# Performance work log

Measured on AMD Instinct MI355X. Metric: run time of the kernel, lower is better.

## Reference

```python
import jax, jax.numpy as jnp
import numpy as np

B, T, N = 128, 32, 196
E = 1024   # embed dim
FD = 1024  # feature dim
H = 1024   # hidden size
A = 1024   # attention dim
SCALE = 0.02


def setup_inputs() -> dict:
    key = jax.random.key(0)
    ks = jax.random.split(key, 16)
    g = lambda k, shape: (jax.random.normal(k, shape, dtype=jnp.float32) * SCALE)
    return {
        "feats": jax.random.normal(ks[0], (B, N, FD), dtype=jnp.float32),
        "embeddings": jax.random.normal(ks[1], (B, T, E), dtype=jnp.float32),
        # additive attention params: v^T tanh(feats @ Wf + h @ Wh + b_att)
        "Wf": g(ks[2], (FD, A)),
        "Wh": g(ks[3], (H, A)),
        "b_att": jnp.zeros((A,), dtype=jnp.float32),
        "v": g(ks[4], (A,)),
        # layer-0 LSTMCell (input = concat(embed, attn) of size E+FD)
        "W_ih0": g(ks[5], (4 * H, E + FD)),
        "W_hh0": g(ks[6], (4 * H, H)),
        "b_ih0": jnp.zeros((4 * H,), dtype=jnp.float32),
        "b_hh0": jnp.zeros((4 * H,), dtype=jnp.float32),
        # layer-1 LSTMCell (input size H)
        "W_ih1": g(ks[7], (4 * H, H)),
        "W_hh1": g(ks[8], (4 * H, H)),
        "b_ih1": jnp.zeros((4 * H,), dtype=jnp.float32),
        "b_hh1": jnp.zeros((4 * H,), dtype=jnp.float32),
    }


def _lstm_cell(x, h, c, W_ih, W_hh, b_ih, b_hh):
    # PyTorch LSTMCell: gates ordered i, f, g, o
    gates = x @ W_ih.T + h @ W_hh.T + (b_ih + b_hh)
    i, f, g, o = jnp.split(gates, 4, axis=-1)
    c_new = jax.nn.sigmoid(f) * c + jax.nn.sigmoid(i) * jnp.tanh(g)
    h_new = jax.nn.sigmoid(o) * jnp.tanh(c_new)
    return h_new, c_new


def reference(feats, embeddings, Wf, Wh, b_att, v, W_ih0, W_hh0, b_ih0, b_hh0,
              W_ih1, W_hh1, b_ih1, b_hh1):
    Bb = embeddings.shape[0]
    # precompute the h-independent half of the attention energies: [B, N, A]
    f_proj = jnp.einsum("bnf,fa->bna", feats, Wf) + b_att

    h0 = jnp.zeros((Bb, H), dtype=feats.dtype)
    c0 = jnp.zeros((Bb, H), dtype=feats.dtype)

    def step(carry, embed_t):
        h0, c0 = carry
        # additive attention with query h0
        e = jnp.tanh(f_proj + (h0 @ Wh)[:, None, :])      # [B, N, A]
        scores = jnp.einsum("bna,a->bn", e, v)            # [B, N]
        alpha = jax.nn.softmax(scores, axis=-1)
        attn = jnp.einsum("bn,bnf->bf", alpha, feats)     # [B, FD]
        x = jnp.concatenate([embed_t, attn], axis=1)      # [B, E+FD]
        h0n, c0n = _lstm_cell(x, h0, c0, W_ih0, W_hh0, b_ih0, b_hh0)
        # faithful to source: layer 1 uses (h0n, c0n) as its state AND h0n as input
        h1, c1 = _lstm_cell(h0n, h0n, c0n, W_ih1, W_hh1, b_ih1, b_hh1)
        return (h0n, c0n), h1

    (_, _), outs = jax.lax.scan(step, (h0, c0), jnp.swapaxes(embeddings, 0, 1))
    return jnp.swapaxes(outs, 0, 1)  # [B, T, H]
```

## Files before the change

kernel.cpp:

```cpp
#include <hip/hip_runtime.h>
#include <cstddef>

typedef unsigned short ushort_t;
typedef unsigned int uint_t;
typedef __attribute__((ext_vector_type(8))) short bf16x8;
typedef __attribute__((ext_vector_type(4))) float f32x4;

constexpr int kB  = 128;
constexpr int kT  = 32;
constexpr int kN  = 196;
constexpr int kH  = 1024;

__device__ __forceinline__ float fsigmoid(float x) { return 1.f / (1.f + __expf(-x)); }
__device__ __forceinline__ float ftanh(float x)    { return 1.f - 2.f / (__expf(2.f * x) + 1.f); }
__device__ __forceinline__ ushort_t f2bf(float f) {
    uint_t u = __float_as_uint(f);
    return (ushort_t)((u + 0x7fffu + ((u >> 16) & 1u)) >> 16);
}

__global__ __launch_bounds__(256) void wf_transpose(
    const float* __restrict__ Wsrc, ushort_t* __restrict__ dst)
{
    __shared__ float t[64][65];
    const int k0 = blockIdx.x * 64, a0 = blockIdx.y * 64;
    const int c = threadIdx.x & 15, r0 = threadIdx.x >> 4;
#pragma unroll
    for (int i = 0; i < 4; ++i) {
        const int r = r0 + i * 16;
        const float4 v = *(const float4*)(Wsrc + (size_t)(k0 + r) * 1024 + a0 + c * 4);
        t[r][c * 4 + 0] = v.x; t[r][c * 4 + 1] = v.y;
        t[r][c * 4 + 2] = v.z; t[r][c * 4 + 3] = v.w;
    }
    __syncthreads();
#pragma unroll
    for (int i = 0; i < 4; ++i) {
        const int r = r0 + i * 16;
        ushort4 h;
        h.x = f2bf(t[c * 4 + 0][r]); h.y = f2bf(t[c * 4 + 1][r]);
        h.z = f2bf(t[c * 4 + 2][r]); h.w = f2bf(t[c * 4 + 3][r]);
        *(ushort4*)&dst[(size_t)(a0 + r) * 1024 + k0 + c * 4] = h;
    }
}

__global__ __launch_bounds__(256) void pack_whh0(
    const float* __restrict__ Whh0, ushort_t* __restrict__ Wbig)
{
    const int idx = blockIdx.x * 256 + threadIdx.x;
    const int j = idx >> 8, k4 = (idx & 255) * 4;
    const int u = j >> 2, g = j & 3;
    const float4 v = *(const float4*)(Whh0 + (size_t)(g * 1024 + u) * 1024 + k4);
    ushort4 h;
    h.x = f2bf(v.x); h.y = f2bf(v.y); h.z = f2bf(v.z); h.w = f2bf(v.w);
    *(ushort4*)&Wbig[(size_t)(1024 + j) * 1024 + k4] = h;
}

__global__ __launch_bounds__(256) void pack_w1sum(
    const float* __restrict__ Wih1, const float* __restrict__ Whh1,
    ushort_t* __restrict__ Wbig)
{
    const int idx = blockIdx.x * 256 + threadIdx.x;
    const int j = idx >> 8, k4 = (idx & 255) * 4;
    const int u = j >> 2, g = j & 3;
    const size_t o = (size_t)(g * 1024 + u) * 1024 + k4;
    const float4 a = *(const float4*)(Wih1 + o);
    const float4 b = *(const float4*)(Whh1 + o);
    ushort4 h;
    h.x = f2bf(a.x + b.x); h.y = f2bf(a.y + b.y);
    h.z = f2bf(a.z + b.z); h.w = f2bf(a.w + b.w);
    *(ushort4*)&Wbig[(size_t)(5120 + j) * 1024 + k4] = h;
}

__global__ __launch_bounds__(256) void pack_w0cat(
    const float* __restrict__ Wih0, ushort_t* __restrict__ W0cat)
{
    const int idx = blockIdx.x * 256 + threadIdx.x;
    const int j = idx >> 9, k4 = (idx & 511) * 4;
    const int u = j >> 2, g = j & 3;
    const int srccol = (k4 < 1024) ? (k4 + 1024) : (k4 - 1024);
    const float4 v = *(const float4*)(Wih0 + (size_t)(g * 1024 + u) * 2048 + srccol);
    ushort4 h;
    h.x = f2bf(v.x); h.y = f2bf(v.y); h.z = f2bf(v.z); h.w = f2bf(v.w);
    *(ushort4*)&W0cat[(size_t)j * 2048 + k4] = h;
}

__global__ __launch_bounds__(256) void cast_bf(
    const float* __restrict__ src, ushort_t* __restrict__ dst)
{
    const size_t idx = ((size_t)blockIdx.x * 256 + threadIdx.x) * 4;
    const float4 v = *(const float4*)(src + idx);
    ushort4 h;
    h.x = f2bf(v.x); h.y = f2bf(v.y); h.z = f2bf(v.z); h.w = f2bf(v.w);
    *(ushort4*)&dst[idx] = h;
}

template<int BF>
__global__ __launch_bounds__(256) void fproj_mfma(
    const float* __restrict__ featsf, const ushort_t* __restrict__ featsbf,
    const ushort_t* __restrict__ WfT,
    const float* __restrict__ bias, ushort_t* __restrict__ fprojbf)
{
    __shared__ ushort_t As[2][128 * 40];
    __shared__ ushort_t Bs[2][128 * 40];

    const int tid = threadIdx.x;
    const int n0 = blockIdx.x * 128, m0 = blockIdx.y * 128;
    const int lane = tid & 63, w = tid >> 6;
    const int wm = (w & 1) * 64, wn = (w >> 1) * 64;
    const int lr = lane & 15, quad = lane >> 4;

    const int xrow0 = tid >> 2, xrow1 = 64 + (tid >> 2);
    const int xkc = (tid & 3) * 8;

    f32x4 acc[4][4];
#pragma unroll
    for (int i = 0; i < 4; ++i)
#pragma unroll
        for (int j = 0; j < 4; ++j)
            acc[i][j] = (f32x4){0.f, 0.f, 0.f, 0.f};

    uint4 a0r, a1r, b0r, b1r;
    float4 f00, f01, f10, f11;

    auto LOAD = [&](int k0) {
        if (BF) {
            a0r = *(const uint4*)&featsbf[(size_t)(m0 + xrow0) * 1024 + k0 + xkc];
            a1r = *(const uint4*)&featsbf[(size_t)(m0 + xrow1) * 1024 + k0 + xkc];
        } else {
            f00 = *(const float4*)&featsf[(size_t)(m0 + xrow0) * 1024 + k0 + xkc];
            f01 = *(const float4*)&featsf[(size_t)(m0 + xrow0) * 1024 + k0 + xkc + 4];
            f10 = *(const float4*)&featsf[(size_t)(m0 + xrow1) * 1024 + k0 + xkc];
            f11 = *(const float4*)&featsf[(size_t)(m0 + xrow1) * 1024 + k0 + xkc + 4];
        }
        b0r = *(const uint4*)&WfT[(size_t)(n0 + xrow0) * 1024 + k0 + xkc];
        b1r = *(const uint4*)&WfT[(size_t)(n0 + xrow1) * 1024 + k0 + xkc];
    };
    auto WRITE = [&](int buf) {
        if (BF) {
            *(uint4*)&As[buf][xrow0 * 40 + xkc] = a0r;
            *(uint4*)&As[buf][xrow1 * 40 + xkc] = a1r;
        } else {
            ushort4 h;
            h.x = f2bf(f00.x); h.y = f2bf(f00.y); h.z = f2bf(f00.z); h.w = f2bf(f00.w);
            *(ushort4*)&As[buf][xrow0 * 40 + xkc] = h;
            h.x = f2bf(f01.x); h.y = f2bf(f01.y); h.z = f2bf(f01.z); h.w = f2bf(f01.w);
            *(ushort4*)&As[buf][xrow0 * 40 + xkc + 4] = h;
            h.x = f2bf(f10.x); h.y = f2bf(f10.y); h.z = f2bf(f10.z); h.w = f2bf(f10.w);
            *(ushort4*)&As[buf][xrow1 * 40 + xkc] = h;
            h.x = f2bf(f11.x); h.y = f2bf(f11.y); h.z = f2bf(f11.z); h.w = f2bf(f11.w);
            *(ushort4*)&As[buf][xrow1 * 40 + xkc + 4] = h;
        }
        *(uint4*)&Bs[buf][xrow0 * 40 + xkc] = b0r;
        *(uint4*)&Bs[buf][xrow1 * 40 + xkc] = b1r;
    };

    LOAD(0); WRITE(0); __syncthreads();
    int cur = 0;
    for (int k0 = 32; k0 <= 1024; k0 += 32) {
        const bool more = (k0 < 1024);
        if (more) LOAD(k0);
        bf16x8 af[4], bb[4];
#pragma unroll
        for (int mf = 0; mf < 4; ++mf)
            af[mf] = *(const bf16x8*)&As[cur][(wm + mf * 16 + lr) * 40 + quad * 8];
#pragma unroll
        for (int nf = 0; nf < 4; ++nf)
            bb[nf] = *(const bf16x8*)&Bs[cur][(wn + nf * 16 + lr) * 40 + quad * 8];
#pragma unroll
        for (int mf = 0; mf < 4; ++mf)
#pragma unroll
            for (int nf = 0; nf < 4; ++nf)
                acc[mf][nf] = __builtin_amdgcn_mfma_f32_16x16x32_bf16(
                    af[mf], bb[nf], acc[mf][nf], 0, 0, 0);
        if (more) WRITE(cur ^ 1);
        __syncthreads();
        cur ^= 1;
    }

#pragma unroll
    for (int nf = 0; nf < 4; ++nf) {
        const int n = n0 + wn + nf * 16 + lr;
        const float bn = bias[n];
#pragma unroll
        for (int mf = 0; mf < 4; ++mf) {
#pragma unroll
            for (int r = 0; r < 4; ++r) {
                const int m = m0 + wm + mf * 16 + quad * 4 + r;
                fprojbf[(size_t)m * 1024 + n] = f2bf(acc[mf][nf][r] + bn);
            }
        }
    }
}

__global__ __launch_bounds__(256) void hgemm_A(
    const ushort_t* __restrict__ hbf, const ushort_t* __restrict__ Wbig,
    const float* __restrict__ cbuf,
    const float* __restrict__ bih1, const float* __restrict__ bhh1,
    float* __restrict__ hwh, float* __restrict__ Ypart,
    float* __restrict__ out, int tstep)
{
    __shared__ ushort_t xs[2][128 * 40];
    __shared__ ushort_t wsB[2][64 * 40];
    __shared__ float eps[128][65];

    const int tid = threadIdx.x;
    const int n0 = blockIdx.x * 64;
    const int lane = tid & 63, w = tid >> 6;
    const int wm = (w & 1) * 64, wn = (w >> 1) * 32;
    const int lr = lane & 15, quad = lane >> 4;

    const int xrow0 = tid >> 2, xrow1 = 64 + (tid >> 2);
    const int xkc = (tid & 3) * 8;

    f32x4 acc[4][2];
#pragma unroll
    for (int i = 0; i < 4; ++i) {
        acc[i][0] = (f32x4){0.f, 0.f, 0.f, 0.f};
        acc[i][1] = (f32x4){0.f, 0.f, 0.f, 0.f};
    }

    uint4 x0r, x1r, w0r;
    auto LOAD = [&](int k0) {
        x0r = *(const uint4*)&hbf[(size_t)xrow0 * 1024 + k0 + xkc];
        x1r = *(const uint4*)&hbf[(size_t)xrow1 * 1024 + k0 + xkc];
        w0r = *(const uint4*)&Wbig[(size_t)(n0 + xrow0) * 1024 + k0 + xkc];
    };
    auto WRITE = [&](int buf) {
        *(uint4*)&xs[buf][xrow0 * 40 + xkc] = x0r;
        *(uint4*)&xs[buf][xrow1 * 40 + xkc] = x1r;
        *(uint4*)&wsB[buf][xrow0 * 40 + xkc] = w0r;
    };

    LOAD(0); WRITE(0); __syncthreads();
    int cur = 0;
    for (int k0 = 32; k0 <= 1024; k0 += 32) {
        const bool more = (k0 < 1024);
        if (more) LOAD(k0);
        bf16x8 af[4], bb[2];
#pragma unroll
        for (int mf = 0; mf < 4; ++mf)
            af[mf] = *(const bf16x8*)&xs[cur][(wm + mf * 16 + lr) * 40 + quad * 8];
#pragma unroll
        for (int nf = 0; nf < 2; ++nf)
            bb[nf] = *(const bf16x8*)&wsB[cur][(wn + nf * 16 + lr) * 40 + quad * 8];
#pragma unroll
        for (int mf = 0; mf < 4; ++mf)
#pragma unroll
            for (int nf = 0; nf < 2; ++nf)
                acc[mf][nf] = __builtin_amdgcn_mfma_f32_16x16x32_bf16(
                    af[mf], bb[nf], acc[mf][nf], 0, 0, 0);
        if (more) WRITE(cur ^ 1);
        __syncthreads();
        cur ^= 1;
    }

    if (n0 < 5120) {
        float* dst = (n0 < 1024) ? hwh : Ypart;
        const int stride = (n0 < 1024) ? 1024 : 4096;
        const int nbase = (n0 < 1024) ? n0 : (n0 - 1024);
#pragma unroll
        for (int mf = 0; mf < 4; ++mf)
#pragma unroll
            for (int nf = 0; nf < 2; ++nf)
#pragma unroll
                for (int r = 0; r < 4; ++r) {
                    const int m = wm + mf * 16 + quad * 4 + r;
                    const int n = nbase + wn + nf * 16 + lr;
                    dst[(size_t)m * stride + n] = acc[mf][nf][r];
                }
    } else {
#pragma unroll
        for (int mf = 0; mf < 4; ++mf)
#pragma unroll
            for (int nf = 0; nf < 2; ++nf)
#pragma unroll
                for (int r = 0; r < 4; ++r)
                    eps[wm + mf * 16 + quad * 4 + r][wn + nf * 16 + lr] = acc[mf][nf][r];
        __syncthreads();
        if (tstep >= 1) {
#pragma unroll
            for (int i = 0; i < 8; ++i) {
                const int cid = i * 256 + tid;
                const int b = cid & 127, ulc = cid >> 7;
                const int u = ((n0 - 5120) >> 2) + ulc;
                const float iv = fsigmoid(eps[b][ulc * 4 + 0] + bih1[u]        + bhh1[u]);
                const float fv = fsigmoid(eps[b][ulc * 4 + 1] + bih1[1024 + u] + bhh1[1024 + u]);
                const float gv = ftanh   (eps[b][ulc * 4 + 2] + bih1[2048 + u] + bhh1[2048 + u]);
                const float ov = fsigmoid(eps[b][ulc * 4 + 3] + bih1[3072 + u] + bhh1[3072 + u]);
                const float cp = cbuf[(size_t)b * 1024 + u];
                const float cn = fv * cp + iv * gv;
                out[((size_t)b * kT + (tstep - 1)) * 1024 + u] = ov * ftanh(cn);
            }
        }
    }
}

__global__ __launch_bounds__(256) void scores_kernel(
    const ushort_t* __restrict__ fprojbf, const float* __restrict__ hwh,
    const float* __restrict__ vvec, float* __restrict__ scoresbuf)
{
    const int b = blockIdx.x, chunk = blockIdx.y;
    const int tid = threadIdx.x, lane = tid & 63, w = tid >> 6;

    float hw[16], vr[16];
    {
        const int a0 = lane * 16;
#pragma unroll
        for (int q = 0; q < 4; ++q) {
            const float4 s0 = *(const float4*)(hwh + (size_t)b * 1024 + a0 + q * 4);
            hw[q * 4 + 0] = s0.x; hw[q * 4 + 1] = s0.y;
            hw[q * 4 + 2] = s0.z; hw[q * 4 + 3] = s0.w;
            const float4 vv = *(const float4*)(vvec + a0 + q * 4);
            vr[q * 4 + 0] = vv.x; vr[q * 4 + 1] = vv.y;
            vr[q * 4 + 2] = vv.z; vr[q * 4 + 3] = vv.w;
        }
    }

#pragma unroll
    for (int i = 0; i < 7; ++i) {
        const int n = chunk * 28 + w * 7 + i;
        const ushort_t* fp = fprojbf + ((size_t)(b * kN + n)) * 1024 + lane * 16;
        const uint4 u0 = *(const uint4*)(fp);
        const uint4 u1 = *(const uint4*)(fp + 8);
        float p = 0.f;
        const uint_t uu[8] = {u0.x, u0.y, u0.z, u0.w, u1.x, u1.y, u1.z, u1.w};
#pragma unroll
        for (int q = 0; q < 8; ++q) {
            const float xa = __uint_as_float(uu[q] << 16);
            const float xb = __uint_as_float(uu[q] & 0xffff0000u);
            p += ftanh(xa + hw[2 * q]) * vr[2 * q];
            p += ftanh(xb + hw[2 * q + 1]) * vr[2 * q + 1];
        }
#pragma unroll
        for (int off = 32; off; off >>= 1) p += __shfl_down(p, off);
        if (lane == 0) scoresbuf[b * kN + n] = p;
    }
}

template<int BF>
__global__ __launch_bounds__(256) void attn_kernel(
    const float* __restrict__ scoresbuf, const float* __restrict__ featsf,
    const ushort_t* __restrict__ featsbf, ushort_t* __restrict__ attnbf)
{
    __shared__ float alpha_s[200];
    __shared__ float red[8];
    const int b = blockIdx.x;
    const int tid = threadIdx.x;

    const float val = (tid < kN) ? scoresbuf[b * kN + tid] : -1e30f;
    float m = val;
#pragma unroll
    for (int off = 32; off; off >>= 1) m = fmaxf(m, __shfl_down(m, off));
    if ((tid & 63) == 0) red[tid >> 6] = m;
    __syncthreads();
    m = fmaxf(fmaxf(red[0], red[1]), fmaxf(red[2], red[3]));
    const float e = (tid < kN) ? __expf(val - m) : 0.f;
    float s = e;
#pragma unroll
    for (int off = 32; off; off >>= 1) s += __shfl_down(s, off);
    if ((tid & 63) == 0) red[4 + (tid >> 6)] = s;
    __syncthreads();
    s = red[4] + red[5] + red[6] + red[7];
    if (tid < kN) alpha_s[tid] = e * (1.f / s);
    __syncthreads();

    if (BF) {
        const int f0 = blockIdx.y * 512 + tid * 2;
        const ushort_t* fb = featsbf + (size_t)b * kN * 1024 + f0;
        float a0 = 0.f, a1 = 0.f;
#pragma unroll 4
        for (int n = 0; n < kN; ++n) {
            const uint_t u = *(const uint_t*)(fb + (size_t)n * 1024);
            a0 += alpha_s[n] * __uint_as_float(u << 16);
            a1 += alpha_s[n] * __uint_as_float(u & 0xffff0000u);
        }
        uint_t o = ((uint_t)f2bf(a1) << 16) | (uint_t)f2bf(a0);
        *(uint_t*)&attnbf[(size_t)b * 1024 + f0] = o;
    } else {
        const int f = blockIdx.y * 256 + tid;
        const float* fb = featsf + (size_t)b * kN * 1024 + f;
        float a = 0.f;
#pragma unroll 4
        for (int n = 0; n < kN; ++n) a += alpha_s[n] * fb[(size_t)n * 1024];
        attnbf[(size_t)b * 1024 + f] = f2bf(a);
    }
}

__global__ __launch_bounds__(256) void gatesC(
    const ushort_t* __restrict__ attnbf, const ushort_t* __restrict__ embbf,
    const ushort_t* __restrict__ W0cat, const float* __restrict__ Ypart,
    const float* __restrict__ bih0, const float* __restrict__ bhh0,
    float* __restrict__ cbuf, ushort_t* __restrict__ hbf, int tstep)
{
    __shared__ ushort_t xs[2][128 * 40];
    __shared__ ushort_t ws2[2][32 * 40];
    __shared__ float eps[128][33];

    const int tid = threadIdx.x;
    const int n0 = blockIdx.x * 32;
    const int lane = tid & 63, w = tid >> 6;
    const int wm = (w & 1) * 64, wn = (w >> 1) * 16;
    const int lr = lane & 15, quad = lane >> 4;

    const int xrow0 = tid >> 2, xrow1 = 64 + (tid >> 2);
    const int xkc = (tid & 3) * 8;
    const int wrow = tid >> 3, wkc = (tid & 7) * 4;

    f32x4 acc[4];
#pragma unroll
    for (int i = 0; i < 4; ++i) acc[i] = (f32x4){0.f, 0.f, 0.f, 0.f};

    uint4 x0r, x1r; uint2 w0r;
    auto LOAD = [&](int k0) {
        const ushort_t* s0 = (k0 < 1024)
            ? (attnbf + (size_t)xrow0 * 1024 + k0)
            : (embbf + ((size_t)xrow0 * kT + tstep) * 1024 + (k0 - 1024));
        const ushort_t* s1 = (k0 < 1024)
            ? (attnbf + (size_t)xrow1 * 1024 + k0)
            : (embbf + ((size_t)xrow1 * kT + tstep) * 1024 + (k0 - 1024));
        x0r = *(const uint4*)(s0 + xkc);
        x1r = *(const uint4*)(s1 + xkc);
        w0r = *(const uint2*)&W0cat[(size_t)(n0 + wrow) * 2048 + k0 + wkc];
    };
    auto WRITE = [&](int buf) {
        *(uint4*)&xs[buf][xrow0 * 40 + xkc] = x0r;
        *(uint4*)&xs[buf][xrow1 * 40 + xkc] = x1r;
        *(uint2*)&ws2[buf][wrow * 40 + wkc] = w0r;
    };

    LOAD(0); WRITE(0); __syncthreads();
    int cur = 0;
    for (int k0 = 32; k0 <= 2048; k0 += 32) {
        const bool more = (k0 < 2048);
        if (more) LOAD(k0);
        bf16x8 af[4], bb;
#pragma unroll
        for (int mf = 0; mf < 4; ++mf)
            af[mf] = *(const bf16x8*)&xs[cur][(wm + mf * 16 + lr) * 40 + quad * 8];
        bb = *(const bf16x8*)&ws2[cur][(wn + lr) * 40 + quad * 8];
#pragma unroll
        for (int mf = 0; mf < 4; ++mf)
            acc[mf] = __builtin_amdgcn_mfma_f32_16x16x32_bf16(
                af[mf], bb, acc[mf], 0, 0, 0);
        if (more) WRITE(cur ^ 1);
        __syncthreads();
        cur ^= 1;
    }

#pragma unroll
    for (int mf = 0; mf < 4; ++mf)
#pragma unroll
        for (int r = 0; r < 4; ++r)
            eps[wm + mf * 16 + quad * 4 + r][wn + lr] = acc[mf][r];
    __syncthreads();

#pragma unroll
    for (int i = 0; i < 4; ++i) {
        const int cid = i * 256 + tid;
        const int b = cid & 127, ulc = cid >> 7;
        const int u = (n0 >> 2) + ulc;
        const int jb = n0 + ulc * 4;
        const float* yp = Ypart + (size_t)b * 4096 + jb;
        const float iv = fsigmoid(eps[b][ulc * 4 + 0] + yp[0] + bih0[u]        + bhh0[u]);
        const float fv = fsigmoid(eps[b][ulc * 4 + 1] + yp[1] + bih0[1024 + u] + bhh0[1024 + u]);
        const float gv = ftanh   (eps[b][ulc * 4 + 2] + yp[2] + bih0[2048 + u] + bhh0[2048 + u]);
        const float ov = fsigmoid(eps[b][ulc * 4 + 3] + yp[3] + bih0[3072 + u] + bhh0[3072 + u]);
        const float cp = cbuf[(size_t)b * 1024 + u];
        const float cn = fv * cp + iv * gv;
        cbuf[(size_t)b * 1024 + u] = cn;
        hbf[(size_t)b * 1024 + u] = f2bf(ov * ftanh(cn));
    }
}

extern "C" void kernel_launch(void* const* d_in, const int* in_sizes, int n_in,
                              void* d_out, int out_size, void* d_ws, size_t ws_size,
                              hipStream_t stream)
{
    const float* feats = (const float*)d_in[0];
    const float* emb   = (const float*)d_in[1];
    const float* Wf    = (const float*)d_in[2];
    const float* Wh    = (const float*)d_in[3];
    const float* b_att = (const float*)d_in[4];
    const float* vvec  = (const float*)d_in[5];
    const float* Wih0  = (const float*)d_in[6];
    const float* Whh0  = (const float*)d_in[7];
    const float* bih0  = (const float*)d_in[8];
    const float* bhh0  = (const float*)d_in[9];
    const float* Wih1  = (const float*)d_in[10];
    const float* Whh1  = (const float*)d_in[11];
    const float* bih1  = (const float*)d_in[12];
    const float* bhh1  = (const float*)d_in[13];
    float* out = (float*)d_out;

    ushort_t* fprojbf = (ushort_t*)d_ws;
    ushort_t* embbf   = fprojbf + (size_t)25088 * 1024;
    ushort_t* Wbig    = embbf   + (size_t)4096 * 1024;
    ushort_t* W0cat   = Wbig    + (size_t)9216 * 1024;
    ushort_t* WfT     = W0cat   + (size_t)4096 * 2048;
    ushort_t* hbf     = WfT     + (size_t)1024 * 1024;
    ushort_t* attnbf  = hbf     + (size_t)128 * 1024;
    float* hwh        = (float*)(attnbf + (size_t)128 * 1024);
    float* Ypart      = hwh   + (size_t)128 * 1024;
    float* cbuf       = Ypart + (size_t)128 * 4096;
    float* scoresbuf  = cbuf  + (size_t)128 * 1024;
    ushort_t* featsbf = (ushort_t*)(scoresbuf + 128 * 196);

    const size_t need_full = 152668160;
    const bool use_bf = (ws_size >= need_full);

    hipMemsetAsync(hbf, 0, sizeof(ushort_t) * 128 * 1024, stream);
    hipMemsetAsync(cbuf, 0, sizeof(float) * 128 * 1024, stream);

    wf_transpose<<<dim3(16, 16), 256, 0, stream>>>(Wf, WfT);
    wf_transpose<<<dim3(16, 16), 256, 0, stream>>>(Wh, Wbig);
    pack_whh0<<<4096, 256, 0, stream>>>(Whh0, Wbig);
    pack_w1sum<<<4096, 256, 0, stream>>>(Wih1, Whh1, Wbig);
    pack_w0cat<<<8192, 256, 0, stream>>>(Wih0, W0cat);
    cast_bf<<<4096, 256, 0, stream>>>(emb, embbf);
    if (use_bf) cast_bf<<<25088, 256, 0, stream>>>(feats, featsbf);

    if (use_bf)
        fproj_mfma<1><<<dim3(8, 196), 256, 0, stream>>>(feats, featsbf, WfT, b_att, fprojbf);
    else
        fproj_mfma<0><<<dim3(8, 196), 256, 0, stream>>>(feats, featsbf, WfT, b_att, fprojbf);

    for (int t = 0; t < kT; ++t) {
        hgemm_A<<<144, 256, 0, stream>>>(hbf, Wbig, cbuf, bih1, bhh1,
                                         hwh, Ypart, out, t);
        scores_kernel<<<dim3(128, 7), 256, 0, stream>>>(fprojbf, hwh, vvec, scoresbuf);
        if (use_bf)
            attn_kernel<1><<<dim3(128, 2), 256, 0, stream>>>(scoresbuf, feats, featsbf, attnbf);
        else
            attn_kernel<0><<<dim3(128, 4), 256, 0, stream>>>(scoresbuf, feats, featsbf, attnbf);
        gatesC<<<128, 256, 0, stream>>>(attnbf, embbf, W0cat, Ypart,
                                        bih0, bhh0, cbuf, hbf, t);
    }
    hgemm_A<<<144, 256, 0, stream>>>(hbf, Wbig, cbuf, bih1, bhh1,
                                     hwh, Ypart, out, kT);

    (void)in_sizes; (void)n_in; (void)out_size; (void)ws_size;
}
```

Baseline: 3.228 ms.

## Fuse per-timestep recurrent kernels into one persistent cooperative kernel with grid sync

```diff
diff --git a/kernel.cpp b/kernel.cpp
--- a/kernel.cpp
+++ b/kernel.cpp
@@ -1,4 +1,5 @@
 #include <hip/hip_runtime.h>
+#include <hip/hip_cooperative_groups.h>
 #include <cstddef>
 
 typedef unsigned short ushort_t;
@@ -10,6 +11,8 @@
 constexpr int kT  = 32;
 constexpr int kN  = 196;
 constexpr int kH  = 1024;
+
+constexpr int ARENA_BYTES = 34816;
 
 __device__ __forceinline__ float fsigmoid(float x) { return 1.f / (1.f + __expf(-x)); }
 __device__ __forceinline__ float ftanh(float x)    { return 1.f - 2.f / (__expf(2.f * x) + 1.f); }
@@ -99,8 +102,10 @@
     const ushort_t* __restrict__ WfT,
     const float* __restrict__ bias, ushort_t* __restrict__ fprojbf)
 {
-    __shared__ ushort_t As[2][128 * 40];
-    __shared__ ushort_t Bs[2][128 * 40];
+    __shared__ alignas(16) char farena[40960];
+    ushort_t* As = (ushort_t*)farena;
+    ushort_t* Bs = As + 2 * 5120;
+    ushort_t* Cs = (ushort_t*)farena;
 
     const int tid = threadIdx.x;
     const int n0 = blockIdx.x * 128, m0 = blockIdx.y * 128;
@@ -136,21 +141,21 @@
     };
     auto WRITE = [&](int buf) {
         if (BF) {
-            *(uint4*)&As[buf][xrow0 * 40 + xkc] = a0r;
-            *(uint4*)&As[buf][xrow1 * 40 + xkc] = a1r;
+            *(uint4*)&As[buf * 5120 + xrow0 * 40 + xkc] = a0r;
+            *(uint4*)&As[buf * 5120 + xrow1 * 40 + xkc] = a1r;
         } else {
             ushort4 h;
             h.x = f2bf(f00.x); h.y = f2bf(f00.y); h.z = f2bf(f00.z); h.w = f2bf(f00.w);
-            *(ushort4*)&As[buf][xrow0 * 40 + xkc] = h;
+            *(ushort4*)&As[buf * 5120 + xrow0 * 40 + xkc] = h;
             h.x = f2bf(f01.x); h.y = f2bf(f01.y); h.z = f2bf(f01.z); h.w = f2bf(f01.w);
-            *(ushort4*)&As[buf][xrow0 * 40 + xkc + 4] = h;
+            *(ushort4*)&As[buf * 5120 + xrow0 * 40 + xkc + 4] = h;
             h.x = f2bf(f10.x); h.y = f2bf(f10.y); h.z = f2bf(f10.z); h.w = f2bf(f10.w);
-            *(ushort4*)&As[buf][xrow1 * 40 + xkc] = h;
+            *(ushort4*)&As[buf * 5120 + xrow1 * 40 + xkc] = h;
             h.x = f2bf(f11.x); h.y = f2bf(f11.y); h.z = f2bf(f11.z); h.w = f2bf(f11.w);
-            *(ushort4*)&As[buf][xrow1 * 40 + xkc + 4] = h;
-        }
-        *(uint4*)&Bs[buf][xrow0 * 40 + xkc] = b0r;
-        *(uint4*)&Bs[buf][xrow1 * 40 + xkc] = b1r;
+            *(ushort4*)&As[buf * 5120 + xrow1 * 40 + xkc + 4] = h;
+        }
+        *(uint4*)&Bs[buf * 5120 + xrow0 * 40 + xkc] = b0r;
+        *(uint4*)&Bs[buf * 5120 + xrow1 * 40 + xkc] = b1r;
     };
 
     LOAD(0); WRITE(0); __syncthreads();
@@ -161,10 +166,10 @@
         bf16x8 af[4], bb[4];
 #pragma unroll
         for (int mf = 0; mf < 4; ++mf)
-            af[mf] = *(const bf16x8*)&As[cur][(wm + mf * 16 + lr) * 40 + quad * 8];
+            af[mf] = *(const bf16x8*)&As[cur * 5120 + (wm + mf * 16 + lr) * 40 + quad * 8];
 #pragma unroll
         for (int nf = 0; nf < 4; ++nf)
-            bb[nf] = *(const bf16x8*)&Bs[cur][(wn + nf * 16 + lr) * 40 + quad * 8];
+            bb[nf] = *(const bf16x8*)&Bs[cur * 5120 + (wn + nf * 16 + lr) * 40 + quad * 8];
 #pragma unroll
         for (int mf = 0; mf < 4; ++mf)
 #pragma unroll
@@ -178,32 +183,40 @@
 
 #pragma unroll
     for (int nf = 0; nf < 4; ++nf) {
-        const int n = n0 + wn + nf * 16 + lr;
-        const float bn = bias[n];
-#pragma unroll
-        for (int mf = 0; mf < 4; ++mf) {
+        const int n = wn + nf * 16 + lr;
+        const float bn = bias[n0 + n];
+#pragma unroll
+        for (int mf = 0; mf < 4; ++mf)
 #pragma unroll
             for (int r = 0; r < 4; ++r) {
-                const int m = m0 + wm + mf * 16 + quad * 4 + r;
-                fprojbf[(size_t)m * 1024 + n] = f2bf(acc[mf][nf][r] + bn);
+                const int m = wm + mf * 16 + quad * 4 + r;
+                Cs[m * 136 + n] = f2bf(acc[mf][nf][r] + bn);
             }
-        }
-    }
-}
-
-__global__ __launch_bounds__(256) void hgemm_A(
+    }
+    __syncthreads();
+#pragma unroll
+    for (int p = 0; p < 8; ++p) {
+        const int row = p * 16 + (tid >> 4);
+        const int c8 = (tid & 15) * 8;
+        const uint4 v = *(const uint4*)&Cs[row * 136 + c8];
+        *(uint4*)&fprojbf[(size_t)(m0 + row) * 1024 + n0 + c8] = v;
+    }
+}
+
+__device__ __forceinline__ void phase_hgemm(
+    char* arena, int job, int tstep,
     const ushort_t* __restrict__ hbf, const ushort_t* __restrict__ Wbig,
     const float* __restrict__ cbuf,
     const float* __restrict__ bih1, const float* __restrict__ bhh1,
     float* __restrict__ hwh, float* __restrict__ Ypart,
-    float* __restrict__ out, int tstep)
-{
-    __shared__ ushort_t xs[2][128 * 40];
-    __shared__ ushort_t wsB[2][64 * 40];
-    __shared__ float eps[128][65];
+    float* __restrict__ out)
+{
+    ushort_t* xs  = (ushort_t*)arena;
+    ushort_t* wsB = xs + 10240;
+    float*    eps = (float*)arena;
 
     const int tid = threadIdx.x;
-    const int n0 = blockIdx.x * 64;
+    const int n0 = job * 64;
     const int lane = tid & 63, w = tid >> 6;
     const int wm = (w & 1) * 64, wn = (w >> 1) * 32;
     const int lr = lane & 15, quad = lane >> 4;
@@ -225,9 +238,9 @@
         w0r = *(const uint4*)&Wbig[(size_t)(n0 + xrow0) * 1024 + k0 + xkc];
     };
     auto WRITE = [&](int buf) {
-        *(uint4*)&xs[buf][xrow0 * 40 + xkc] = x0r;
-        *(uint4*)&xs[buf][xrow1 * 40 + xkc] = x1r;
-        *(uint4*)&wsB[buf][xrow0 * 40 + xkc] = w0r;
+        *(uint4*)&xs[buf * 5120 + xrow0 * 40 + xkc] = x0r;
+        *(uint4*)&xs[buf * 5120 + xrow1 * 40 + xkc] = x1r;
+        *(uint4*)&wsB[buf * 2560 + xrow0 * 40 + xkc] = w0r;
     };
 
     LOAD(0); WRITE(0); __syncthreads();
@@ -238,10 +251,10 @@
         bf16x8 af[4], bb[2];
 #pragma unroll
         for (int mf = 0; mf < 4; ++mf)
-            af[mf] = *(const bf16x8*)&xs[cur][(wm + mf * 16 + lr) * 40 + quad * 8];
+            af[mf] = *(const bf16x8*)&xs[cur * 5120 + (wm + mf * 16 + lr) * 40 + quad * 8];
 #pragma unroll
         for (int nf = 0; nf < 2; ++nf)
-            bb[nf] = *(const bf16x8*)&wsB[cur][(wn + nf * 16 + lr) * 40 + quad * 8];
+            bb[nf] = *(const bf16x8*)&wsB[cur * 2560 + (wn + nf * 16 + lr) * 40 + quad * 8];
 #pragma unroll
         for (int mf = 0; mf < 4; ++mf)
 #pragma unroll
@@ -274,7 +287,7 @@
             for (int nf = 0; nf < 2; ++nf)
 #pragma unroll
                 for (int r = 0; r < 4; ++r)
-                    eps[wm + mf * 16 + quad * 4 + r][wn + nf * 16 + lr] = acc[mf][nf][r];
+                    eps[(wm + mf * 16 + quad * 4 + r) * 65 + (wn + nf * 16 + lr)] = acc[mf][nf][r];
         __syncthreads();
         if (tstep >= 1) {
 #pragma unroll
@@ -282,10 +295,10 @@
                 const int cid = i * 256 + tid;
                 const int b = cid & 127, ulc = cid >> 7;
                 const int u = ((n0 - 5120) >> 2) + ulc;
-                const float iv = fsigmoid(eps[b][ulc * 4 + 0] + bih1[u]        + bhh1[u]);
-                const float fv = fsigmoid(eps[b][ulc * 4 + 1] + bih1[1024 + u] + bhh1[1024 + u]);
-                const float gv = ftanh   (eps[b][ulc * 4 + 2] + bih1[2048 + u] + bhh1[2048 + u]);
-                const float ov = fsigmoid(eps[b][ulc * 4 + 3] + bih1[3072 + u] + bhh1[3072 + u]);
+                const float iv = fsigmoid(eps[b * 65 + ulc * 4 + 0] + bih1[u]        + bhh1[u]);
+                const float fv = fsigmoid(eps[b * 65 + ulc * 4 + 1] + bih1[1024 + u] + bhh1[1024 + u]);
+                const float gv = ftanh   (eps[b * 65 + ulc * 4 + 2] + bih1[2048 + u] + bhh1[2048 + u]);
+                const float ov = fsigmoid(eps[b * 65 + ulc * 4 + 3] + bih1[3072 + u] + bhh1[3072 + u]);
                 const float cp = cbuf[(size_t)b * 1024 + u];
                 const float cn = fv * cp + iv * gv;
                 out[((size_t)b * kT + (tstep - 1)) * 1024 + u] = ov * ftanh(cn);
@@ -294,11 +307,12 @@
     }
 }
 
-__global__ __launch_bounds__(256) void scores_kernel(
+__device__ __forceinline__ void phase_scores(
+    int job,
     const ushort_t* __restrict__ fprojbf, const float* __restrict__ hwh,
     const float* __restrict__ vvec, float* __restrict__ scoresbuf)
 {
-    const int b = blockIdx.x, chunk = blockIdx.y;
+    const int b = job & 127, chunk = job >> 7;
     const int tid = threadIdx.x, lane = tid & 63, w = tid >> 6;
 
     float hw[16], vr[16];
@@ -336,14 +350,14 @@
     }
 }
 
-template<int BF>
-__global__ __launch_bounds__(256) void attn_kernel(
-    const float* __restrict__ scoresbuf, const float* __restrict__ featsf,
-    const ushort_t* __restrict__ featsbf, ushort_t* __restrict__ attnbf)
-{
-    __shared__ float alpha_s[200];
-    __shared__ float red[8];
-    const int b = blockIdx.x;
+__device__ __forceinline__ void phase_attn(
+    char* arena, int job,
+    const float* __restrict__ scoresbuf, const ushort_t* __restrict__ featsbf,
+    ushort_t* __restrict__ attnbf)
+{
+    float* alpha_s = (float*)arena;
+    float* red = alpha_s + 200;
+    const int b = job >> 1;
     const int tid = threadIdx.x;
 
     const float val = (tid < kN) ? scoresbuf[b * kN + tid] : -1e30f;
@@ -363,40 +377,32 @@
     if (tid < kN) alpha_s[tid] = e * (1.f / s);
     __syncthreads();
 
-    if (BF) {
-        const int f0 = blockIdx.y * 512 + tid * 2;
-        const ushort_t* fb = featsbf + (size_t)b * kN * 1024 + f0;
-        float a0 = 0.f, a1 = 0.f;
+    const int f0 = (job & 1) * 512 + tid * 2;
+    const ushort_t* fb = featsbf + (size_t)b * kN * 1024 + f0;
+    float a0 = 0.f, a1 = 0.f;
 #pragma unroll 4
-        for (int n = 0; n < kN; ++n) {
-            const uint_t u = *(const uint_t*)(fb + (size_t)n * 1024);
-            a0 += alpha_s[n] * __uint_as_float(u << 16);
-            a1 += alpha_s[n] * __uint_as_float(u & 0xffff0000u);
-        }
-        uint_t o = ((uint_t)f2bf(a1) << 16) | (uint_t)f2bf(a0);
-        *(uint_t*)&attnbf[(size_t)b * 1024 + f0] = o;
-    } else {
-        const int f = blockIdx.y * 256 + tid;
-        const float* fb = featsf + (size_t)b * kN * 1024 + f;
-        float a = 0.f;
-#pragma unroll 4
-        for (int n = 0; n < kN; ++n) a += alpha_s[n] * fb[(size_t)n * 1024];
-        attnbf[(size_t)b * 1024 + f] = f2bf(a);
-    }
-}
-
-__global__ __launch_bounds__(256) void gatesC(
+    for (int n = 0; n < kN; ++n) {
+        const uint_t u = *(const uint_t*)(fb + (size_t)n * 1024);
+        a0 += alpha_s[n] * __uint_as_float(u << 16);
+        a1 += alpha_s[n] * __uint_as_float(u & 0xffff0000u);
+    }
+    uint_t o = ((uint_t)f2bf(a1) << 16) | (uint_t)f2bf(a0);
+    *(uint_t*)&attnbf[(size_t)b * 1024 + f0] = o;
+}
+
+__device__ __forceinline__ void phase_gates(
+    char* arena, int job, int tstep,
     const ushort_t* __restrict__ attnbf, const ushort_t* __restrict__ embbf,
     const ushort_t* __restrict__ W0cat, const float* __restrict__ Ypart,
     const float* __restrict__ bih0, const float* __restrict__ bhh0,
-    float* __restrict__ cbuf, ushort_t* __restrict__ hbf, int tstep)
-{
-    __shared__ ushort_t xs[2][128 * 40];
-    __shared__ ushort_t ws2[2][32 * 40];
-    __shared__ float eps[128][33];
+    float* __restrict__ cbuf, ushort_t* __restrict__ hbf)
+{
+    ushort_t* xs  = (ushort_t*)arena;
+    ushort_t* ws2 = xs + 10240;
+    float*    eps = (float*)arena;
 
     const int tid = threadIdx.x;
-    const int n0 = blockIdx.x * 32;
+    const int n0 = job * 32;
     const int lane = tid & 63, w = tid >> 6;
     const int wm = (w & 1) * 64, wn = (w >> 1) * 16;
     const int lr = lane & 15, quad = lane >> 4;
@@ -422,9 +428,9 @@
         w0r = *(const uint2*)&W0cat[(size_t)(n0 + wrow) * 2048 + k0 + wkc];
     };
     auto WRITE = [&](int buf) {
-        *(uint4*)&xs[buf][xrow0 * 40 + xkc] = x0r;
-        *(uint4*)&xs[buf][xrow1 * 40 + xkc] = x1r;
-        *(uint2*)&ws2[buf][wrow * 40 + wkc] = w0r;
+        *(uint4*)&xs[buf * 5120 + xrow0 * 40 + xkc] = x0r;
+        *(uint4*)&xs[buf * 5120 + xrow1 * 40 + xkc] = x1r;
+        *(uint2*)&ws2[buf * 1280 + wrow * 40 + wkc] = w0r;
     };
 
     LOAD(0); WRITE(0); __syncthreads();
@@ -435,8 +441,8 @@
         bf16x8 af[4], bb;
 #pragma unroll
         for (int mf = 0; mf < 4; ++mf)
-            af[mf] = *(const bf16x8*)&xs[cur][(wm + mf * 16 + lr) * 40 + quad * 8];
-        bb = *(const bf16x8*)&ws2[cur][(wn + lr) * 40 + quad * 8];
+            af[mf] = *(const bf16x8*)&xs[cur * 5120 + (wm + mf * 16 + lr) * 40 + quad * 8];
+        bb = *(const bf16x8*)&ws2[cur * 1280 + (wn + lr) * 40 + quad * 8];
 #pragma unroll
         for (int mf = 0; mf < 4; ++mf)
             acc[mf] = __builtin_amdgcn_mfma_f32_16x16x32_bf16(
@@ -450,7 +456,7 @@
     for (int mf = 0; mf < 4; ++mf)
 #pragma unroll
         for (int r = 0; r < 4; ++r)
-            eps[wm + mf * 16 + quad * 4 + r][wn + lr] = acc[mf][r];
+            eps[(wm + mf * 16 + quad * 4 + r) * 33 + wn + lr] = acc[mf][r];
     __syncthreads();
 
 #pragma unroll
@@ -460,15 +466,125 @@
         const int u = (n0 >> 2) + ulc;
         const int jb = n0 + ulc * 4;
         const float* yp = Ypart + (size_t)b * 4096 + jb;
-        const float iv = fsigmoid(eps[b][ulc * 4 + 0] + yp[0] + bih0[u]        + bhh0[u]);
-        const float fv = fsigmoid(eps[b][ulc * 4 + 1] + yp[1] + bih0[1024 + u] + bhh0[1024 + u]);
-        const float gv = ftanh   (eps[b][ulc * 4 + 2] + yp[2] + bih0[2048 + u] + bhh0[2048 + u]);
-        const float ov = fsigmoid(eps[b][ulc * 4 + 3] + yp[3] + bih0[3072 + u] + bhh0[3072 + u]);
+        const float iv = fsigmoid(eps[b * 33 + ulc * 4 + 0] + yp[0] + bih0[u]        + bhh0[u]);
+        const float fv = fsigmoid(eps[b * 33 + ulc * 4 + 1] + yp[1] + bih0[1024 + u] + bhh0[1024 + u]);
+        const float gv = ftanh   (eps[b * 33 + ulc * 4 + 2] + yp[2] + bih0[2048 + u] + bhh0[2048 + u]);
+        const float ov = fsigmoid(eps[b * 33 + ulc * 4 + 3] + yp[3] + bih0[3072 + u] + bhh0[3072 + u]);
         const float cp = cbuf[(size_t)b * 1024 + u];
         const float cn = fv * cp + iv * gv;
         cbuf[(size_t)b * 1024 + u] = cn;
         hbf[(size_t)b * 1024 + u] = f2bf(ov * ftanh(cn));
     }
+}
+
+__global__ __launch_bounds__(256) void hgemm_A(
+    const ushort_t* __restrict__ hbf, const ushort_t* __restrict__ Wbig,
+    const float* __restrict__ cbuf,
+    const float* __restrict__ bih1, const float* __restrict__ bhh1,
+    float* __restrict__ hwh, float* __restrict__ Ypart,
+    float* __restrict__ out, int tstep)
+{
+    __shared__ alignas(16) char arena[ARENA_BYTES];
+    phase_hgemm(arena, blockIdx.x, tstep, hbf, Wbig, cbuf, bih1, bhh1, hwh, Ypart, out);
+}
+
+__global__ __launch_bounds__(256) void scores_kernel(
+    const ushort_t* __restrict__ fprojbf, const float* __restrict__ hwh,
+    const float* __restrict__ vvec, float* __restrict__ scoresbuf)
+{
+    phase_scores(blockIdx.x + 128 * blockIdx.y, fprojbf, hwh, vvec, scoresbuf);
+}
+
+template<int BF>
+__global__ __launch_bounds__(256) void attn_kernel(
+    const float* __restrict__ scoresbuf, const float* __restrict__ featsf,
+    const ushort_t* __restrict__ featsbf, ushort_t* __restrict__ attnbf)
+{
+    __shared__ float alpha_s[200];
+    __shared__ float red[8];
+    const int b = blockIdx.x;
+    const int tid = threadIdx.x;
+
+    const float val = (tid < kN) ? scoresbuf[b * kN + tid] : -1e30f;
+    float m = val;
+#pragma unroll
+    for (int off = 32; off; off >>= 1) m = fmaxf(m, __shfl_down(m, off));
+    if ((tid & 63) == 0) red[tid >> 6] = m;
+    __syncthreads();
+    m = fmaxf(fmaxf(red[0], red[1]), fmaxf(red[2], red[3]));
+    const float e = (tid < kN) ? __expf(val - m) : 0.f;
+    float s = e;
+#pragma unroll
+    for (int off = 32; off; off >>= 1) s += __shfl_down(s, off);
+    if ((tid & 63) == 0) red[4 + (tid >> 6)] = s;
+    __syncthreads();
+    s = red[4] + red[5] + red[6] + red[7];
+    if (tid < kN) alpha_s[tid] = e * (1.f / s);
+    __syncthreads();
+
+    if (BF) {
+        const int f0 = blockIdx.y * 512 + tid * 2;
+        const ushort_t* fb = featsbf + (size_t)b * kN * 1024 + f0;
+        float a0 = 0.f, a1 = 0.f;
+#pragma unroll 4
+        for (int n = 0; n < kN; ++n) {
+            const uint_t u = *(const uint_t*)(fb + (size_t)n * 1024);
+            a0 += alpha_s[n] * __uint_as_float(u << 16);
+            a1 += alpha_s[n] * __uint_as_float(u & 0xffff0000u);
+        }
+        uint_t o = ((uint_t)f2bf(a1) << 16) | (uint_t)f2bf(a0);
+        *(uint_t*)&attnbf[(size_t)b * 1024 + f0] = o;
+    } else {
+        const int f = blockIdx.y * 256 + tid;
+        const float* fb = featsf + (size_t)b * kN * 1024 + f;
+        float a = 0.f;
+#pragma unroll 4
+        for (int n = 0; n < kN; ++n) a += alpha_s[n] * fb[(size_t)n * 1024];
+        attnbf[(size_t)b * 1024 + f] = f2bf(a);
+    }
+}
+
+__global__ __launch_bounds__(256) void gatesC(
+    const ushort_t* __restrict__ attnbf, const ushort_t* __restrict__ embbf,
+    const ushort_t* __restrict__ W0cat, const float* __restrict__ Ypart,
+    const float* __restrict__ bih0, const float* __restrict__ bhh0,
+    float* __restrict__ cbuf, ushort_t* __restrict__ hbf, int tstep)
+{
+    __shared__ alignas(16) char arena[ARENA_BYTES];
+    phase_gates(arena, blockIdx.x, tstep, attnbf, embbf, W0cat, Ypart,
+                bih0, bhh0, cbuf, hbf);
+}
+
+__global__ __launch_bounds__(256, 2) void mega_kernel(
+    ushort_t* hbf, const ushort_t* Wbig, float* cbuf,
+    const float* bih1, const float* bhh1,
+    float* hwh, float* Ypart, float* out,
+    const ushort_t* fprojbf, const float* vvec, float* scoresbuf,
+    const ushort_t* featsbf, ushort_t* attnbf,
+    const ushort_t* embbf, const ushort_t* W0cat,
+    const float* bih0, const float* bhh0)
+{
+    __shared__ alignas(16) char arena[ARENA_BYTES];
+    cooperative_groups::grid_group grid = cooperative_groups::this_grid();
+    const int blk = blockIdx.x;
+
+    for (int t = 0; t < kT; ++t) {
+        if (blk < 144)
+            phase_hgemm(arena, blk, t, hbf, Wbig, cbuf, bih1, bhh1, hwh, Ypart, out);
+        grid.sync();
+        for (int j = blk; j < 896; j += 512)
+            phase_scores(j, fprojbf, hwh, vvec, scoresbuf);
+        grid.sync();
+        if (blk < 256)
+            phase_attn(arena, blk, scoresbuf, featsbf, attnbf);
+        grid.sync();
+        if (blk < 128)
+            phase_gates(arena, blk, t, attnbf, embbf, W0cat, Ypart,
+                        bih0, bhh0, cbuf, hbf);
+        grid.sync();
+    }
+    if (blk < 64)
+        phase_hgemm(arena, 80 + blk, kT, hbf, Wbig, cbuf, bih1, bhh1, hwh, Ypart, out);
 }
 
 extern "C" void kernel_launch(void* const* d_in, const int* in_sizes, int n_in,
@@ -523,19 +639,47 @@
     else
         fproj_mfma<0><<<dim3(8, 196), 256, 0, stream>>>(feats, featsbf, WfT, b_att, fprojbf);
 
-    for (int t = 0; t < kT; ++t) {
+    bool did_coop = false;
+    if (use_bf) {
+        static int coop_ok = -1;
+        if (coop_ok < 0) {
+            int dev = 0; (void)hipGetDevice(&dev);
+            int coop = 0;
+            (void)hipDeviceGetAttribute(&coop, hipDeviceAttributeCooperativeLaunch, dev);
+            int ncu = 0;
+            (void)hipDeviceGetAttribute(&ncu, hipDeviceAttributeMultiprocessorCount, dev);
+            int maxb = 0;
+            hipError_t oe = hipOccupancyMaxActiveBlocksPerMultiprocessor(
+                &maxb, mega_kernel, 256, 0);
+            coop_ok = (coop != 0 && oe == hipSuccess && (long)maxb * ncu >= 512) ? 1 : 0;
+        }
+        if (coop_ok) {
+            void* kargs[] = {
+                (void*)&hbf, (void*)&Wbig, (void*)&cbuf, (void*)&bih1, (void*)&bhh1,
+                (void*)&hwh, (void*)&Ypart, (void*)&out, (void*)&fprojbf, (void*)&vvec,
+                (void*)&scoresbuf, (void*)&featsbf, (void*)&attnbf, (void*)&embbf,
+                (void*)&W0cat, (void*)&bih0, (void*)&bhh0 };
+            hipError_t le = hipLaunchCooperativeKernel(
+                mega_kernel, dim3(512), dim3(256), kargs, 0u, stream);
+            did_coop = (le == hipSuccess);
+        }
+    }
+
+    if (!did_coop) {
+        for (int t = 0; t < kT; ++t) {
+            hgemm_A<<<144, 256, 0, stream>>>(hbf, Wbig, cbuf, bih1, bhh1,
+                                             hwh, Ypart, out, t);
+            scores_kernel<<<dim3(128, 7), 256, 0, stream>>>(fprojbf, hwh, vvec, scoresbuf);
+            if (use_bf)
+                attn_kernel<1><<<dim3(128, 2), 256, 0, stream>>>(scoresbuf, feats, featsbf, attnbf);
+            else
+                attn_kernel<0><<<dim3(128, 4), 256, 0, stream>>>(scoresbuf, feats, featsbf, attnbf);
+            gatesC<<<128, 256, 0, stream>>>(attnbf, embbf, W0cat, Ypart,
+                                            bih0, bhh0, cbuf, hbf, t);
+        }
         hgemm_A<<<144, 256, 0, stream>>>(hbf, Wbig, cbuf, bih1, bhh1,
-                                         hwh, Ypart, out, t);
-        scores_kernel<<<dim3(128, 7), 256, 0, stream>>>(fprojbf, hwh, vvec, scoresbuf);
-        if (use_bf)
-            attn_kernel<1><<<dim3(128, 2), 256, 0, stream>>>(scoresbuf, feats, featsbf, attnbf);
-        else
-            attn_kernel<0><<<dim3(128, 4), 256, 0, stream>>>(scoresbuf, feats, featsbf, attnbf);
-        gatesC<<<128, 256, 0, stream>>>(attnbf, embbf, W0cat, Ypart,
-                                        bih0, bhh0, cbuf, hbf, t);
-    }
-    hgemm_A<<<144, 256, 0, stream>>>(hbf, Wbig, cbuf, bih1, bhh1,
-                                     hwh, Ypart, out, kT);
+                                         hwh, Ypart, out, kT);
+    }
 
     (void)in_sizes; (void)n_in; (void)out_size; (void)ws_size;
 }
```

Result: no change. 3.225 ms (-0.1%).
